# Kernel optimization log

Measured on AMD Instinct MI355X. Metric: run time of the kernel, lower is better.

The kernel has to match this reference:

```python
import jax, jax.numpy as jnp
import numpy as np

N_HEAD = 16
QMIN, QMAX = 0.0, 255.0  # 8-bit asymmetric


def fake_quantize(x, scale, zp):
    # LearnableFakeQuantize (asymmetric, 8-bit) with straight-through round.
    q = x / scale + zp
    q = q + jax.lax.stop_gradient(jnp.round(q) - q)  # STE round
    q = jnp.clip(q, QMIN, QMAX)
    return (q - zp) * scale


def setup_inputs() -> dict:
    key = jax.random.key(0)
    ks = jax.random.split(key, 4)
    B, T, C = 2, 2048, 1024
    return {
        "hidden_states": jax.random.normal(ks[0], (B, T, C), jnp.float32),
        "W_attn": jax.random.normal(ks[1], (C, 3 * C), jnp.float32) * (1.0 / np.sqrt(C)),
        "b_attn": jnp.zeros((3 * C,), jnp.float32),
        "W_proj": jax.random.normal(ks[2], (C, C), jnp.float32) * (1.0 / np.sqrt(C)),
        "b_proj": jnp.zeros((C,), jnp.float32),
        "kv_scale": jnp.full((1,), 0.05, jnp.float32),
        "kv_zp": jnp.full((1,), 128.0, jnp.float32),
    }


def reference(hidden_states, W_attn, b_attn, W_proj, b_proj, kv_scale, kv_zp):
    B, T, C = hidden_states.shape
    H = N_HEAD
    D = C // H
    qkv = hidden_states @ W_attn + b_attn            # [B,T,3C]
    q, k, v = jnp.split(qkv, 3, axis=2)
    # [B,T,C] -> [B,H,T,D]
    q = q.reshape(B, T, H, D).transpose(0, 2, 1, 3)
    k = k.reshape(B, T, H, D).transpose(0, 2, 1, 3)
    v = v.reshape(B, T, H, D).transpose(0, 2, 1, 3)
    k = fake_quantize(k, kv_scale, kv_zp)
    v = fake_quantize(v, kv_scale, kv_zp)
    scores = jnp.einsum("bhqd,bhkd->bhqk", q, k) / jnp.sqrt(jnp.asarray(D, q.dtype))
    causal = jnp.tril(jnp.ones((T, T), bool))        # bias[:T,:T]
    scores = jnp.where(causal, scores, jnp.asarray(-jnp.inf, scores.dtype))
    attn = jax.nn.softmax(scores, axis=-1)
    out = jnp.einsum("bhqk,bhkd->bhqd", attn, v)     # [B,H,T,D]
    out = out.transpose(0, 2, 1, 3).reshape(B, T, C)
    return out @ W_proj + b_proj
```

## Files before the change

### kernel.cpp

```cpp
#include <hip/hip_runtime.h>
#include <math.h>

#define TB 2048
#define CC 1024
#define NH 16
#define HD 64

typedef __bf16 bf16x8 __attribute__((ext_vector_type(8)));
typedef __bf16 bf16x4 __attribute__((ext_vector_type(4)));
typedef float  f32x4  __attribute__((ext_vector_type(4)));

__device__ inline float exp2fast(float x) { return __builtin_amdgcn_exp2f(x); }

__device__ __forceinline__ void gl_lds16(const __bf16* g, __bf16* l) {
    __builtin_amdgcn_global_load_lds(
        (const __attribute__((address_space(1))) void*)g,
        (__attribute__((address_space(3))) void*)l, 16, 0, 0);
}

__global__ __launch_bounds__(256)
void cvt_kernel(const float* __restrict__ src, __bf16* __restrict__ dst) {
    int i = (blockIdx.x * 256 + threadIdx.x) * 4;
    f32x4 v = *(const f32x4*)&src[i];
    bf16x4 o;
    o.x = (__bf16)v.x; o.y = (__bf16)v.y; o.z = (__bf16)v.z; o.w = (__bf16)v.w;
    *(bf16x4*)&dst[i] = o;
}

__global__ __launch_bounds__(256)
void tpose_kernel(const float* __restrict__ src, __bf16* __restrict__ dst,
                  int K, int N) {
    __shared__ __bf16 L[64][68];
    const int tid = threadIdx.x;
    const int n0 = blockIdx.x * 64, k0 = blockIdx.y * 64;
    #pragma unroll
    for (int i = 0; i < 4; i++) {
        int id = tid + i * 256;
        int r = id >> 4, c = (id & 15) * 4;
        f32x4 v = *(const f32x4*)&src[(size_t)(k0 + r) * N + n0 + c];
        bf16x4 o;
        o.x = (__bf16)v.x; o.y = (__bf16)v.y; o.z = (__bf16)v.z; o.w = (__bf16)v.w;
        *(bf16x4*)&L[r][c] = o;
    }
    __syncthreads();
    #pragma unroll
    for (int i = 0; i < 4; i++) {
        int id = tid + i * 256;
        int nr = id >> 4, kc = (id & 15) * 4;
        bf16x4 o;
        o.x = L[kc + 0][nr]; o.y = L[kc + 1][nr];
        o.z = L[kc + 2][nr]; o.w = L[kc + 3][nr];
        *(bf16x4*)&dst[(size_t)(n0 + nr) * K + k0 + kc] = o;
    }
}

template<int BN, int MODE>
__global__ __launch_bounds__(256)
void gemm_bt(const __bf16* __restrict__ A, const __bf16* __restrict__ Bt,
             const float* __restrict__ bias,
             __bf16* __restrict__ o0, __bf16* __restrict__ o1,
             __bf16* __restrict__ o2, float* __restrict__ of,
             int M, int N, int K,
             const float* __restrict__ scp, const float* __restrict__ zpp)
{
    constexpr int NT = BN / 32;
    __shared__ __bf16 Asm[128][32];
    __shared__ __bf16 Bsm[BN][32];

    const int tid  = threadIdx.x;
    const int m0   = blockIdx.y * 128;
    const int n0   = blockIdx.x * BN;
    const int w    = tid >> 6, lane = tid & 63;
    const int wm   = (w & 1) * 64, wn = (w >> 1) * (BN / 2);
    const int r16  = lane & 15, quad = lane >> 4;
    const int srow = lane >> 2, scol = (lane & 3) * 8;

    f32x4 acc[4][NT];
    #pragma unroll
    for (int i = 0; i < 4; i++)
        #pragma unroll
        for (int j = 0; j < NT; j++) acc[i][j] = 0.f;

    for (int k0 = 0; k0 < K; k0 += 32) {
        #pragma unroll
        for (int p = 0; p < 2; p++)
            gl_lds16(&A[(size_t)(m0 + p * 64 + w * 16 + srow) * K + k0 + scol],
                     &Asm[p * 64 + w * 16][0]);
        #pragma unroll
        for (int p = 0; p < BN / 64; p++)
            gl_lds16(&Bt[(size_t)(n0 + p * 64 + w * 16 + srow) * K + k0 + scol],
                     &Bsm[p * 64 + w * 16][0]);
        __syncthreads();

        bf16x8 af[4], bfr[NT];
        #pragma unroll
        for (int mt = 0; mt < 4; mt++)
            af[mt] = *(const bf16x8*)&Asm[wm + mt * 16 + r16][quad * 8];
        #pragma unroll
        for (int nt = 0; nt < NT; nt++)
            bfr[nt] = *(const bf16x8*)&Bsm[wn + nt * 16 + r16][quad * 8];
        #pragma unroll
        for (int mt = 0; mt < 4; mt++)
            #pragma unroll
            for (int nt = 0; nt < NT; nt++)
                acc[mt][nt] = __builtin_amdgcn_mfma_f32_16x16x32_bf16(
                    af[mt], bfr[nt], acc[mt][nt], 0, 0, 0);
        __syncthreads();
    }

    const float sc = scp[0];
    const float zp = zpp[0];

    #pragma unroll
    for (int mt = 0; mt < 4; mt++) {
        #pragma unroll
        for (int nt = 0; nt < NT; nt++) {
            #pragma unroll
            for (int r = 0; r < 4; r++) {
                int gm = m0 + wm + mt * 16 + quad * 4 + r;
                int gn = n0 + wn + nt * 16 + r16;
                float val = acc[mt][nt][r] + bias[gn];
                if (MODE == 1) {
                    of[(size_t)gm * N + gn] = val;
                } else {
                    int part = gn >> 10;
                    int idx  = gn & 1023;
                    int h = idx >> 6, d = idx & 63;
                    int b = gm >> 11, t = gm & 2047;
                    size_t off = (((size_t)(b * NH + h)) * TB + t) * HD + d;
                    if (part == 0) {
                        o0[off] = (__bf16)val;
                    } else {
                        float qv = val / sc + zp;
                        qv = rintf(qv);
                        qv = fminf(fmaxf(qv, 0.f), 255.f);
                        float dq = (qv - zp) * sc;
                        if (part == 1) o1[off] = (__bf16)dq;
                        else           o2[off] = (__bf16)dq;
                    }
                }
            }
        }
    }
}

__global__ __launch_bounds__(256)
void attn_mfma(const __bf16* __restrict__ Q, const __bf16* __restrict__ Kg,
               const __bf16* __restrict__ Vg, __bf16* __restrict__ O)
{
    __shared__ alignas(16) __bf16 Ksm[64][72];
    __shared__ alignas(16) __bf16 Vsm[64][72];
    __shared__ alignas(16) __bf16 Psm[4][16][72];

    const int tid  = threadIdx.x;
    const int qt   = 31 - (blockIdx.x >> 5);
    const int bh   = blockIdx.x & 31;
    const int q0   = qt * 64;
    const int w    = tid >> 6, lane = tid & 63;
    const int l15  = lane & 15, quad = lane >> 4;
    const int b    = bh >> 4, h = bh & 15;

    const float cs = 0.125f * 1.44269504f;

    const __bf16* Qrow = Q + ((size_t)bh * TB + q0 + w * 16 + l15) * HD;
    bf16x8 qf[2];
    qf[0] = *(const bf16x8*)&Qrow[quad * 8];
    qf[1] = *(const bf16x8*)&Qrow[32 + quad * 8];

    f32x4 acc_o[4];
    #pragma unroll
    for (int nt = 0; nt < 4; nt++) acc_o[nt] = 0.f;
    f32x4 mrun, lrun;
    #pragma unroll
    for (int r = 0; r < 4; r++) { mrun[r] = -3.0e38f; lrun[r] = 0.f; }

    const __bf16* Kbh = Kg + (size_t)bh * TB * HD;
    const __bf16* Vbh = Vg + (size_t)bh * TB * HD;

    for (int kt = 0; kt <= qt; kt++) {
        __syncthreads();
        #pragma unroll
        for (int i = 0; i < 2; i++) {
            int id = tid + i * 256;
            int row = id >> 3, c = id & 7;
            *(bf16x8*)&Ksm[row][c * 8] =
                *(const bf16x8*)&Kbh[(size_t)(kt * 64 + row) * HD + c * 8];
        }
        #pragma unroll
        for (int i = 0; i < 2; i++) {
            int id = tid + i * 256;
            int key = id & 63, c = id >> 6;
            bf16x8 v = *(const bf16x8*)&Vbh[(size_t)(kt * 64 + key) * HD + c * 8];
            #pragma unroll
            for (int j = 0; j < 8; j++) Vsm[c * 8 + j][key] = v[j];
        }
        __syncthreads();

        const bool diag = (kt == qt);

        f32x4 s[4];
        #pragma unroll
        for (int nt = 0; nt < 4; nt++) s[nt] = 0.f;
        #pragma unroll
        for (int nt = 0; nt < 4; nt++) {
            if (diag && nt > w) continue;
            #pragma unroll
            for (int ks = 0; ks < 2; ks++) {
                bf16x8 kf = *(const bf16x8*)&Ksm[nt * 16 + l15][ks * 32 + quad * 8];
                s[nt] = __builtin_amdgcn_mfma_f32_16x16x32_bf16(qf[ks], kf, s[nt], 0, 0, 0);
            }
        }
        #pragma unroll
        for (int nt = 0; nt < 4; nt++)
            #pragma unroll
            for (int r = 0; r < 4; r++) s[nt][r] *= cs;

        const int rowb = w * 16 + quad * 4;
        if (diag) {
            #pragma unroll
            for (int nt = 0; nt < 4; nt++) {
                int keyl = nt * 16 + l15;
                #pragma unroll
                for (int r = 0; r < 4; r++)
                    if (keyl > rowb + r) s[nt][r] = -3.0e38f;
            }
        }

        f32x4 mx = s[0];
        #pragma unroll
        for (int nt = 1; nt < 4; nt++)
            #pragma unroll
            for (int r = 0; r < 4; r++) mx[r] = fmaxf(mx[r], s[nt][r]);
        #pragma unroll
        for (int mk = 1; mk < 16; mk <<= 1)
            #pragma unroll
            for (int r = 0; r < 4; r++)
                mx[r] = fmaxf(mx[r], __shfl_xor(mx[r], mk));

        f32x4 mnew, alpha;
        #pragma unroll
        for (int r = 0; r < 4; r++) {
            mnew[r]  = fmaxf(mrun[r], mx[r]);
            alpha[r] = exp2fast(mrun[r] - mnew[r]);
        }
        #pragma unroll
        for (int nt = 0; nt < 4; nt++)
            #pragma unroll
            for (int r = 0; r < 4; r++) acc_o[nt][r] *= alpha[r];

        f32x4 ls;
        #pragma unroll
        for (int r = 0; r < 4; r++) ls[r] = 0.f;
        #pragma unroll
        for (int nt = 0; nt < 4; nt++)
            #pragma unroll
            for (int r = 0; r < 4; r++) {
                float p = exp2fast(s[nt][r] - mnew[r]);
                s[nt][r] = p;
                ls[r] += p;
            }
        #pragma unroll
        for (int mk = 1; mk < 16; mk <<= 1)
            #pragma unroll
            for (int r = 0; r < 4; r++) ls[r] += __shfl_xor(ls[r], mk);
        #pragma unroll
        for (int r = 0; r < 4; r++) lrun[r] = lrun[r] * alpha[r] + ls[r];
        mrun = mnew;

        #pragma unroll
        for (int nt = 0; nt < 4; nt++)
            #pragma unroll
            for (int r = 0; r < 4; r++)
                Psm[w][quad * 4 + r][nt * 16 + l15] = (__bf16)s[nt][r];
        asm volatile("s_waitcnt lgkmcnt(0)" ::: "memory");

        bf16x8 pf0 = *(const bf16x8*)&Psm[w][l15][quad * 8];
        bf16x8 pf1 = *(const bf16x8*)&Psm[w][l15][32 + quad * 8];
        #pragma unroll
        for (int nt = 0; nt < 4; nt++) {
            bf16x8 vf0 = *(const bf16x8*)&Vsm[nt * 16 + l15][quad * 8];
            bf16x8 vf1 = *(const bf16x8*)&Vsm[nt * 16 + l15][32 + quad * 8];
            acc_o[nt] = __builtin_amdgcn_mfma_f32_16x16x32_bf16(pf0, vf0, acc_o[nt], 0, 0, 0);
            acc_o[nt] = __builtin_amdgcn_mfma_f32_16x16x32_bf16(pf1, vf1, acc_o[nt], 0, 0, 0);
        }
    }

    f32x4 inv;
    #pragma unroll
    for (int r = 0; r < 4; r++) inv[r] = 1.f / lrun[r];
    #pragma unroll
    for (int nt = 0; nt < 4; nt++)
        #pragma unroll
        for (int r = 0; r < 4; r++) {
            size_t row = (size_t)(b * TB) + q0 + w * 16 + quad * 4 + r;
            O[row * CC + h * HD + nt * 16 + l15] = (__bf16)(acc_o[nt][r] * inv[r]);
        }
}

extern "C" void kernel_launch(void* const* d_in, const int* in_sizes, int n_in,
                              void* d_out, int out_size, void* d_ws, size_t ws_size,
                              hipStream_t stream) {
    (void)in_sizes; (void)n_in; (void)out_size; (void)ws_size;
    const float* hidden   = (const float*)d_in[0];
    const float* W_attn   = (const float*)d_in[1];
    const float* b_attn   = (const float*)d_in[2];
    const float* W_proj   = (const float*)d_in[3];
    const float* b_proj   = (const float*)d_in[4];
    const float* kv_scale = (const float*)d_in[5];
    const float* kv_zp    = (const float*)d_in[6];
    float* out = (float*)d_out;

    __bf16* hb  = (__bf16*)d_ws;
    __bf16* wat = hb  + (size_t)4096 * 1024;
    __bf16* wpt = wat + (size_t)3072 * 1024;
    __bf16* qws = wpt + (size_t)1024 * 1024;
    __bf16* kws = qws + (size_t)2 * NH * TB * HD;
    __bf16* vws = kws + (size_t)2 * NH * TB * HD;
    __bf16* ows = vws + (size_t)2 * NH * TB * HD;

    cvt_kernel<<<4096, 256, 0, stream>>>(hidden, hb);
    tpose_kernel<<<dim3(48, 16), 256, 0, stream>>>(W_attn, wat, 1024, 3072);
    tpose_kernel<<<dim3(16, 16), 256, 0, stream>>>(W_proj, wpt, 1024, 1024);

    gemm_bt<128, 0><<<dim3(24, 32), 256, 0, stream>>>(
        hb, wat, b_attn, qws, kws, vws, nullptr, 4096, 3072, 1024, kv_scale, kv_zp);

    attn_mfma<<<dim3(32 * 32), 256, 0, stream>>>(qws, kws, vws, ows);

    gemm_bt<64, 1><<<dim3(16, 32), 256, 0, stream>>>(
        ows, wpt, b_proj, nullptr, nullptr, nullptr, out, 4096, 1024, 1024,
        kv_scale, kv_zp);
}
```

Measured before the change: 221.8 us.

## Transpose attention MFMAs to keep P in registers and prefetch K/V tiles

```diff
diff --git a/kernel.cpp b/kernel.cpp
--- a/kernel.cpp
+++ b/kernel.cpp
@@ -129,7 +129,7 @@
                     int b = gm >> 11, t = gm & 2047;
                     size_t off = (((size_t)(b * NH + h)) * TB + t) * HD + d;
                     if (part == 0) {
-                        o0[off] = (__bf16)val;
+                        o0[off] = (__bf16)(val * 0.18033688f);
                     } else {
                         float qv = val / sc + zp;
                         qv = rintf(qv);
@@ -144,13 +144,12 @@
     }
 }
 
-__global__ __launch_bounds__(256)
+__global__ __launch_bounds__(256, 4)
 void attn_mfma(const __bf16* __restrict__ Q, const __bf16* __restrict__ Kg,
                const __bf16* __restrict__ Vg, __bf16* __restrict__ O)
 {
     __shared__ alignas(16) __bf16 Ksm[64][72];
     __shared__ alignas(16) __bf16 Vsm[64][72];
-    __shared__ alignas(16) __bf16 Psm[4][16][72];
 
     const int tid  = threadIdx.x;
     const int qt   = 31 - (blockIdx.x >> 5);
@@ -160,42 +159,58 @@
     const int l15  = lane & 15, quad = lane >> 4;
     const int b    = bh >> 4, h = bh & 15;
 
-    const float cs = 0.125f * 1.44269504f;
-
-    const __bf16* Qrow = Q + ((size_t)bh * TB + q0 + w * 16 + l15) * HD;
-    bf16x8 qf[2];
-    qf[0] = *(const bf16x8*)&Qrow[quad * 8];
-    qf[1] = *(const bf16x8*)&Qrow[32 + quad * 8];
-
-    f32x4 acc_o[4];
-    #pragma unroll
-    for (int nt = 0; nt < 4; nt++) acc_o[nt] = 0.f;
-    f32x4 mrun, lrun;
-    #pragma unroll
-    for (int r = 0; r < 4; r++) { mrun[r] = -3.0e38f; lrun[r] = 0.f; }
+    const int krow = tid >> 3;
+    const int kseg = (tid & 7) * 8;
+    const int vkey = tid & 63;
+    const int vc   = tid >> 6;
 
     const __bf16* Kbh = Kg + (size_t)bh * TB * HD;
     const __bf16* Vbh = Vg + (size_t)bh * TB * HD;
 
+    const __bf16* Qrow = Q + ((size_t)bh * TB + q0 + w * 16 + l15) * HD;
+    bf16x8 qf0 = *(const bf16x8*)&Qrow[quad * 8];
+    bf16x8 qf1 = *(const bf16x8*)&Qrow[32 + quad * 8];
+
+    const int rbase = (l15 >> 2) * 8 + (l15 & 3);
+
+    bf16x8 af_l;
+    {
+        __bf16 v = (l15 == 0) ? (__bf16)1.0f : (__bf16)0.0f;
+        #pragma unroll
+        for (int j = 0; j < 8; j++) af_l[j] = v;
+    }
+
+    f32x4 acc_o[4], acc_l;
+    #pragma unroll
+    for (int nt = 0; nt < 4; nt++) acc_o[nt] = 0.f;
+    acc_l = 0.f;
+    float mrun = -3.0e38f;
+
+    bf16x8 kpre0 = *(const bf16x8*)&Kbh[(size_t)krow * HD + kseg];
+    bf16x8 kpre1 = *(const bf16x8*)&Kbh[(size_t)(32 + krow) * HD + kseg];
+    bf16x8 vpre0 = *(const bf16x8*)&Vbh[(size_t)vkey * HD + vc * 8];
+    bf16x8 vpre1 = *(const bf16x8*)&Vbh[(size_t)vkey * HD + (4 + vc) * 8];
+
     for (int kt = 0; kt <= qt; kt++) {
         __syncthreads();
-        #pragma unroll
-        for (int i = 0; i < 2; i++) {
-            int id = tid + i * 256;
-            int row = id >> 3, c = id & 7;
-            *(bf16x8*)&Ksm[row][c * 8] =
-                *(const bf16x8*)&Kbh[(size_t)(kt * 64 + row) * HD + c * 8];
-        }
-        #pragma unroll
-        for (int i = 0; i < 2; i++) {
-            int id = tid + i * 256;
-            int key = id & 63, c = id >> 6;
-            bf16x8 v = *(const bf16x8*)&Vbh[(size_t)(kt * 64 + key) * HD + c * 8];
-            #pragma unroll
-            for (int j = 0; j < 8; j++) Vsm[c * 8 + j][key] = v[j];
+        *(bf16x8*)&Ksm[krow][kseg]      = kpre0;
+        *(bf16x8*)&Ksm[32 + krow][kseg] = kpre1;
+        #pragma unroll
+        for (int j = 0; j < 8; j++) {
+            Vsm[vc * 8 + j][vkey]      = vpre0[j];
+            Vsm[32 + vc * 8 + j][vkey] = vpre1[j];
         }
         __syncthreads();
 
+        if (kt < qt) {
+            const __bf16* Kn = Kbh + (size_t)(kt + 1) * 64 * HD;
+            const __bf16* Vn = Vbh + (size_t)(kt + 1) * 64 * HD;
+            kpre0 = *(const bf16x8*)&Kn[(size_t)krow * HD + kseg];
+            kpre1 = *(const bf16x8*)&Kn[(size_t)(32 + krow) * HD + kseg];
+            vpre0 = *(const bf16x8*)&Vn[(size_t)vkey * HD + vc * 8];
+            vpre1 = *(const bf16x8*)&Vn[(size_t)vkey * HD + (4 + vc) * 8];
+        }
+
         const bool diag = (kt == qt);
 
         f32x4 s[4];
@@ -203,98 +218,78 @@
         for (int nt = 0; nt < 4; nt++) s[nt] = 0.f;
         #pragma unroll
         for (int nt = 0; nt < 4; nt++) {
-            if (diag && nt > w) continue;
-            #pragma unroll
-            for (int ks = 0; ks < 2; ks++) {
-                bf16x8 kf = *(const bf16x8*)&Ksm[nt * 16 + l15][ks * 32 + quad * 8];
-                s[nt] = __builtin_amdgcn_mfma_f32_16x16x32_bf16(qf[ks], kf, s[nt], 0, 0, 0);
-            }
-        }
-        #pragma unroll
-        for (int nt = 0; nt < 4; nt++)
-            #pragma unroll
-            for (int r = 0; r < 4; r++) s[nt][r] *= cs;
-
-        const int rowb = w * 16 + quad * 4;
+            if (diag && (nt & 1) && w < 2) continue;
+            int row = rbase + (nt & 1) * 32 + ((nt >> 1) << 2);
+            bf16x8 kf0 = *(const bf16x8*)&Ksm[row][quad * 8];
+            bf16x8 kf1 = *(const bf16x8*)&Ksm[row][32 + quad * 8];
+            s[nt] = __builtin_amdgcn_mfma_f32_16x16x32_bf16(kf0, qf0, s[nt], 0, 0, 0);
+            s[nt] = __builtin_amdgcn_mfma_f32_16x16x32_bf16(kf1, qf1, s[nt], 0, 0, 0);
+        }
+
         if (diag) {
             #pragma unroll
             for (int nt = 0; nt < 4; nt++) {
-                int keyl = nt * 16 + l15;
+                int koff = (nt & 1) * 32 + ((nt >> 1) << 2) + quad * 8;
                 #pragma unroll
                 for (int r = 0; r < 4; r++)
-                    if (keyl > rowb + r) s[nt][r] = -3.0e38f;
+                    if (koff + r > w * 16 + l15) s[nt][r] = -3.0e38f;
             }
         }
 
-        f32x4 mx = s[0];
-        #pragma unroll
-        for (int nt = 1; nt < 4; nt++)
-            #pragma unroll
-            for (int r = 0; r < 4; r++) mx[r] = fmaxf(mx[r], s[nt][r]);
-        #pragma unroll
-        for (int mk = 1; mk < 16; mk <<= 1)
-            #pragma unroll
-            for (int r = 0; r < 4; r++)
-                mx[r] = fmaxf(mx[r], __shfl_xor(mx[r], mk));
-
-        f32x4 mnew, alpha;
-        #pragma unroll
-        for (int r = 0; r < 4; r++) {
-            mnew[r]  = fmaxf(mrun[r], mx[r]);
-            alpha[r] = exp2fast(mrun[r] - mnew[r]);
-        }
+        float mx = s[0][0];
         #pragma unroll
         for (int nt = 0; nt < 4; nt++)
             #pragma unroll
-            for (int r = 0; r < 4; r++) acc_o[nt][r] *= alpha[r];
-
-        f32x4 ls;
-        #pragma unroll
-        for (int r = 0; r < 4; r++) ls[r] = 0.f;
+            for (int r = 0; r < 4; r++) mx = fmaxf(mx, s[nt][r]);
+        mx = fmaxf(mx, __shfl_xor(mx, 16));
+        mx = fmaxf(mx, __shfl_xor(mx, 32));
+
+        float mnew  = fmaxf(mrun, mx);
+        float alpha = exp2fast(mrun - mnew);
+        mrun = mnew;
         #pragma unroll
         for (int nt = 0; nt < 4; nt++)
             #pragma unroll
-            for (int r = 0; r < 4; r++) {
-                float p = exp2fast(s[nt][r] - mnew[r]);
-                s[nt][r] = p;
-                ls[r] += p;
-            }
-        #pragma unroll
-        for (int mk = 1; mk < 16; mk <<= 1)
-            #pragma unroll
-            for (int r = 0; r < 4; r++) ls[r] += __shfl_xor(ls[r], mk);
-        #pragma unroll
-        for (int r = 0; r < 4; r++) lrun[r] = lrun[r] * alpha[r] + ls[r];
-        mrun = mnew;
-
+            for (int r = 0; r < 4; r++) acc_o[nt][r] *= alpha;
+        acc_l[0] *= alpha;
+
+        float p[4][4];
         #pragma unroll
         for (int nt = 0; nt < 4; nt++)
             #pragma unroll
-            for (int r = 0; r < 4; r++)
-                Psm[w][quad * 4 + r][nt * 16 + l15] = (__bf16)s[nt][r];
-        asm volatile("s_waitcnt lgkmcnt(0)" ::: "memory");
-
-        bf16x8 pf0 = *(const bf16x8*)&Psm[w][l15][quad * 8];
-        bf16x8 pf1 = *(const bf16x8*)&Psm[w][l15][32 + quad * 8];
+            for (int r = 0; r < 4; r++) p[nt][r] = exp2fast(s[nt][r] - mnew);
+
+        bf16x8 pf0, pf1;
+        #pragma unroll
+        for (int j = 0; j < 4; j++) {
+            pf0[j]     = (__bf16)p[0][j];
+            pf0[4 + j] = (__bf16)p[2][j];
+            pf1[j]     = (__bf16)p[1][j];
+            pf1[4 + j] = (__bf16)p[3][j];
+        }
+
+        acc_l = __builtin_amdgcn_mfma_f32_16x16x32_bf16(af_l, pf0, acc_l, 0, 0, 0);
+        acc_l = __builtin_amdgcn_mfma_f32_16x16x32_bf16(af_l, pf1, acc_l, 0, 0, 0);
+
         #pragma unroll
         for (int nt = 0; nt < 4; nt++) {
             bf16x8 vf0 = *(const bf16x8*)&Vsm[nt * 16 + l15][quad * 8];
             bf16x8 vf1 = *(const bf16x8*)&Vsm[nt * 16 + l15][32 + quad * 8];
-            acc_o[nt] = __builtin_amdgcn_mfma_f32_16x16x32_bf16(pf0, vf0, acc_o[nt], 0, 0, 0);
-            acc_o[nt] = __builtin_amdgcn_mfma_f32_16x16x32_bf16(pf1, vf1, acc_o[nt], 0, 0, 0);
-        }
-    }
-
-    f32x4 inv;
-    #pragma unroll
-    for (int r = 0; r < 4; r++) inv[r] = 1.f / lrun[r];
-    #pragma unroll
-    for (int nt = 0; nt < 4; nt++)
-        #pragma unroll
-        for (int r = 0; r < 4; r++) {
-            size_t row = (size_t)(b * TB) + q0 + w * 16 + quad * 4 + r;
-            O[row * CC + h * HD + nt * 16 + l15] = (__bf16)(acc_o[nt][r] * inv[r]);
-        }
+            acc_o[nt] = __builtin_amdgcn_mfma_f32_16x16x32_bf16(vf0, pf0, acc_o[nt], 0, 0, 0);
+            acc_o[nt] = __builtin_amdgcn_mfma_f32_16x16x32_bf16(vf1, pf1, acc_o[nt], 0, 0, 0);
+        }
+    }
+
+    float lall = __shfl(acc_l[0], l15);
+    float inv  = 1.f / lall;
+    size_t trow = (size_t)(b * TB) + q0 + w * 16 + l15;
+    #pragma unroll
+    for (int nt = 0; nt < 4; nt++) {
+        bf16x4 st;
+        #pragma unroll
+        for (int r = 0; r < 4; r++) st[r] = (__bf16)(acc_o[nt][r] * inv);
+        *(bf16x4*)&O[trow * CC + h * HD + nt * 16 + quad * 4] = st;
+    }
 }
 
 extern "C" void kernel_launch(void* const* d_in, const int* in_sizes, int n_in,
```

Result: faster. 191.2 us (-13.8%).
